# Optimization experiments

Measured on AMD Instinct MI355X. Metric: run time of the kernel, lower is better.

The kernel has to match this reference:

```python
import jax, jax.numpy as jnp
import numpy as np

MODES1 = 16
MODES2 = 16
WIDTH = 64


def spectral_conv2d(x, w):
    # x: [b, ci, n1, n2] real; w: [ci, co, m1, m2, 2] real (re, im)
    b, ci, n1, n2 = x.shape
    co, m1, m2 = w.shape[1], w.shape[2], w.shape[3]
    x_ft = jnp.fft.rfft2(x, norm='ortho')              # [b, ci, n1, n2//2+1] complex
    wc = w[..., 0] + 1j * w[..., 1]                     # [ci, co, m1, m2]
    blk = jnp.einsum('bixy,ioxy->boxy', x_ft[:, :, :m1, :m2], wc)
    out_ft = jnp.zeros((b, co, n1, n2 // 2 + 1), dtype=x_ft.dtype)
    out_ft = out_ft.at[:, :, :m1, :m2].set(blk)
    return jnp.fft.irfft2(out_ft, s=(n1, n2), norm='ortho')


def conv1x1(x, w, bias):
    # x: [b, ci, n1, n2]; w: [co, ci]; bias: [co]
    return jnp.einsum('bixy,oi->boxy', x, w) + bias[None, :, None, None]


def setup_inputs() -> dict:
    key = jax.random.key(0)
    ks = jax.random.split(key, 20)
    B, CIN, N1, N2 = 16, 3, 256, 256
    W = WIDTH
    scale = 1.0 / (W * W)
    inp = {
        'x': jax.random.normal(ks[0], (B, CIN, N1, N2), dtype=jnp.float32),
        'fc0_w': jax.random.normal(ks[1], (W, CIN), dtype=jnp.float32) * 0.1,
        'fc0_b': jnp.zeros((W,), dtype=jnp.float32),
        'sw1': scale * jax.random.normal(ks[2], (W, W, MODES1, MODES2, 2), dtype=jnp.float32),
        'sw2': scale * jax.random.normal(ks[3], (W, W, MODES1, MODES2, 2), dtype=jnp.float32),
        'sw3': scale * jax.random.normal(ks[4], (W, W, MODES1, MODES2, 2), dtype=jnp.float32),
        'sw4': scale * jax.random.normal(ks[5], (W, W, MODES1, MODES2, 2), dtype=jnp.float32),
        'cw1': jax.random.normal(ks[6], (W, W), dtype=jnp.float32) * 0.05,
        'cb1': jnp.zeros((W,), dtype=jnp.float32),
        'cw2': jax.random.normal(ks[7], (W, W), dtype=jnp.float32) * 0.05,
        'cb2': jnp.zeros((W,), dtype=jnp.float32),
        'cw3': jax.random.normal(ks[8], (W, W), dtype=jnp.float32) * 0.05,
        'cb3': jnp.zeros((W,), dtype=jnp.float32),
        'cw4': jax.random.normal(ks[9], (W, W), dtype=jnp.float32) * 0.05,
        'cb4': jnp.zeros((W,), dtype=jnp.float32),
        'fc1_w': jax.random.normal(ks[10], (64, W), dtype=jnp.float32) * 0.05,
        'fc1_b': jnp.zeros((64,), dtype=jnp.float32),
        'fc2_w': jax.random.normal(ks[11], (1, 64), dtype=jnp.float32) * 0.05,
        'fc2_b': jnp.zeros((1,), dtype=jnp.float32),
    }
    return inp


def reference(x, fc0_w, fc0_b, sw1, sw2, sw3, sw4,
              cw1, cb1, cw2, cb2, cw3, cb3, cw4, cb4,
              fc1_w, fc1_b, fc2_w, fc2_b):
    # lift: [b, c, n1, n2] -> channels-last Linear -> [b, width, n1, n2]
    h = jnp.einsum('bcxy,wc->bwxy', x, fc0_w) + fc0_b[None, :, None, None]
    for sw, cw, cb in ((sw1, cw1, cb1), (sw2, cw2, cb2), (sw3, cw3, cb3), (sw4, cw4, cb4)):
        h = jax.nn.gelu(spectral_conv2d(h, sw) + conv1x1(h, cw, cb), approximate=False)
    # projection head (channels-last linears)
    h = jax.nn.gelu(jnp.einsum('bwxy,fw->bfxy', h, fc1_w) + fc1_b[None, :, None, None], approximate=False)
    out = jnp.einsum('bfxy,of->boxy', h, fc2_w) + fc2_b[None, :, None, None]
    return out
```

## Files before the change

### kernel.cpp

```cpp
#include <hip/hip_runtime.h>
#include <math.h>


typedef unsigned int   u32;
typedef unsigned short u16;
typedef __attribute__((ext_vector_type(8))) __bf16 bf16x8;
typedef __attribute__((ext_vector_type(4))) float  f32x4;

constexpr long F1_B  = 134217728;
constexpr long G_B   = 150994944;
constexpr long F2_B  = 167772160;
constexpr long CC_B  = 169869312;
constexpr long WF_B  = 171966464;
constexpr long WXI_B = 171999232;
constexpr long TWF_B = 172032000;
constexpr long BAS_B = 172048384;
constexpr long WSP_B = 172064768;

constexpr int HOP = 76;

union BU { uint2 u2[2]; uint4 u4; bf16x8 v; u16 s[8]; };

__device__ __forceinline__ float gelu_exact(float v) {
    return 0.5f * v * (1.0f + erff(v * 0.70710678118654752440f));
}
__device__ __forceinline__ float bflo(u32 u) { return __uint_as_float(u << 16); }
__device__ __forceinline__ float bfhi(u32 u) { return __uint_as_float(u & 0xffff0000u); }
__device__ __forceinline__ u16 f2bf(float f) {
    u32 u = __float_as_uint(f);
    u += 0x7fffu + ((u >> 16) & 1u);
    return (u16)(u >> 16);
}
__device__ __forceinline__ u32 pack2bf(float a, float b) {
    return (u32)f2bf(a) | ((u32)f2bf(b) << 16);
}

__global__ __launch_bounds__(256) void k_tab(float* __restrict__ wf,
                                             float* __restrict__ wxi,
                                             u16* __restrict__ twf,
                                             u16* __restrict__ bas) {
    const int t = blockIdx.x * 256 + threadIdx.x;
    if (t < 4096) {
        const int y = t >> 4, k = t & 15;
        const int m = (k * y) & 255;
        double s, c; sincospi((double)m / 128.0, &s, &c);
        wf[t * 2] = (float)c; wf[t * 2 + 1] = (float)(-s);
    } else if (t < 8192) {
        const int u = t - 4096;
        const int k1 = u >> 8, x = u & 255;
        const int m = (k1 * x) & 255;
        double s, c; sincospi((double)m / 128.0, &s, &c);
        wxi[u * 2] = (float)c; wxi[u * 2 + 1] = (float)s;
    } else if (t < 16384) {
        const int u = t - 8192;
        const int kc = u >> 8, y = u & 255;
        const int k2 = kc >> 1;
        const int m = (k2 * y) & 255;
        double s, c; sincospi((double)m / 128.0, &s, &c);
        twf[kc * 256 + y] = f2bf((kc & 1) ? (float)(-s) : (float)c);
    } else {
        const int u = t - 16384;
        const int y = u >> 5, kc = u & 31;
        const int k2 = kc >> 1;
        const int m = (k2 * y) & 255;
        double s, c; sincospi((double)m / 128.0, &s, &c);
        const float cc = (k2 == 0) ? 1.0f : 2.0f;
        bas[y * 32 + kc] = f2bf((kc & 1) ? (float)(-cc * s) : (float)(cc * c));
    }
}

__global__ __launch_bounds__(256) void k_wsplit(const float* __restrict__ c1,
                                                const float* __restrict__ c2,
                                                const float* __restrict__ c3,
                                                const float* __restrict__ c4,
                                                const float* __restrict__ f1w,
                                                u16* __restrict__ wsp) {
    const int t = blockIdx.x * 256 + threadIdx.x;
    const int w = t >> 12, p = t & 4095;
    const float* src = (w == 0) ? c1 : (w == 1) ? c2 : (w == 2) ? c3
                     : (w == 3) ? c4 : f1w;
    const float f = src[p];
    const u16 hi = f2bf(f);
    const u16 lo = f2bf(f - __uint_as_float((u32)hi << 16));
    u16* dst = wsp + w * 8192 + (p >> 6) * 128 + (p & 63);
    dst[0]  = hi;
    dst[64] = lo;
}

__device__ __forceinline__ void f1t_epilogue(const u16* HOyo,
                                             const u16* __restrict__ twf,
                                             u16* __restrict__ f1,
                                             int b, int x, int tid) {
    const int lane = tid & 63, wave = tid >> 6;
    const int quad = lane >> 4, col = lane & 15;
    const int o = wave * 16 + col;
    f32x4 a0 = {0.f, 0.f, 0.f, 0.f}, a1 = {0.f, 0.f, 0.f, 0.f};
    #pragma unroll
    for (int ks = 0; ks < 8; ks++) {
        const int kb = ks * 32 + quad * 8;
        BU bb;
        #pragma unroll
        for (int j = 0; j < 8; j++) bb.s[j] = HOyo[(kb + j) * HOP + o];
        const bf16x8 af0 = *(const bf16x8*)(twf + col * 256 + kb);
        const bf16x8 af1 = *(const bf16x8*)(twf + (16 + col) * 256 + kb);
        a0 = __builtin_amdgcn_mfma_f32_16x16x32_bf16(af0, bb.v, a0, 0, 0, 0);
        a1 = __builtin_amdgcn_mfma_f32_16x16x32_bf16(af1, bb.v, a1, 0, 0, 0);
    }
    u16* dst = f1 + (((long)(b * 64 + o)) * 256 + x) * 32 + quad * 4;
    uint2 w;
    w.x = pack2bf(a0[0], a0[1]); w.y = pack2bf(a0[2], a0[3]);
    *(uint2*)dst = w;
    w.x = pack2bf(a1[0], a1[1]); w.y = pack2bf(a1[2], a1[3]);
    *(uint2*)(dst + 16) = w;
}

__global__ __launch_bounds__(256) void k_lift(const float* __restrict__ xin,
                                              const float* __restrict__ w0,
                                              const float* __restrict__ b0,
                                              u16* __restrict__ h,
                                              const u16* __restrict__ twf,
                                              u16* __restrict__ f1) {
    __shared__ float ws0[192], bs0[64];
    __shared__ u16 HOyo[256 * HOP];
    const int tid = threadIdx.x;
    if (tid < 192) ws0[tid] = w0[tid];
    if (tid < 64)  bs0[tid] = b0[tid];
    __syncthreads();
    const int b = blockIdx.x >> 8, x = blockIdx.x & 255;
    const long pix = (((long)b * 3) * 256 + x) * 256 + tid;
    const float x0 = xin[pix];
    const float x1 = xin[pix + 65536];
    const float x2 = xin[pix + 131072];
    u32 pr[32];
    #pragma unroll
    for (int w = 0; w < 64; w += 2) {
        float v0 = bs0[w], v1 = bs0[w + 1];
        v0 = fmaf(x0, ws0[w * 3],     v0);  v1 = fmaf(x0, ws0[w * 3 + 3], v1);
        v0 = fmaf(x1, ws0[w * 3 + 1], v0);  v1 = fmaf(x1, ws0[w * 3 + 4], v1);
        v0 = fmaf(x2, ws0[w * 3 + 2], v0);  v1 = fmaf(x2, ws0[w * 3 + 5], v1);
        pr[w >> 1] = pack2bf(v0, v1);
    }
    u16* hrow = h + (((long)(b * 256 + x)) << 14) + (long)tid * 64;
    #pragma unroll
    for (int q = 0; q < 8; q++) *(uint4*)(hrow + q * 8) = ((uint4*)pr)[q];
    #pragma unroll
    for (int q = 0; q < 16; q++)
        *(uint2*)(HOyo + tid * HOP + q * 4) = ((uint2*)pr)[q];
    __syncthreads();
    f1t_epilogue(HOyo, twf, f1, b, x, tid);
}

__global__ __launch_bounds__(256) void k_dftx(const u16* __restrict__ f1,
                                              const float* __restrict__ wf,
                                              float* __restrict__ f2) {
    const int tid = threadIdx.x;
    const int k1 = tid >> 4, k2 = tid & 15;
    const u16* base = f1 + (long)blockIdx.x * 8192;
    float cr0 = 0, ci0 = 0, cr1 = 0, ci1 = 0;
    for (int x = 0; x < 256; x += 2) {
        const u32 wa = *(const u32*)(base + x * 32 + k2 * 2);
        const float2 ta = *(const float2*)(wf + x * 32 + k1 * 2);
        const float Far = bflo(wa), Fai = bfhi(wa);
        cr0 = fmaf(Far, ta.x, fmaf(-Fai, ta.y, cr0));
        ci0 = fmaf(Fai, ta.x, fmaf(Far, ta.y, ci0));
        const u32 wb = *(const u32*)(base + (x + 1) * 32 + k2 * 2);
        const float2 tb = *(const float2*)(wf + (x + 1) * 32 + k1 * 2);
        const float Fbr = bflo(wb), Fbi = bfhi(wb);
        cr1 = fmaf(Fbr, tb.x, fmaf(-Fbi, tb.y, cr1));
        ci1 = fmaf(Fbi, tb.x, fmaf(Fbr, tb.y, ci1));
    }
    const int m = k1 * 16 + k2;
    *(float2*)(f2 + ((long)m * 1024 + blockIdx.x) * 2) =
        make_float2(cr0 + cr1, ci0 + ci1);
}

__global__ __launch_bounds__(256) void k_mode(const float* __restrict__ f2,
                                              const float* __restrict__ sw,
                                              float* __restrict__ cc) {
    __shared__ __align__(16) float wsh[8192];
    __shared__ __align__(16) float fsh[2048];
    const int tid = threadIdx.x;
    const int m = blockIdx.x;
    const float scale = 1.0f / 65536.0f;
    for (int p = tid; p < 4096; p += 256) {
        const float2 w = *(const float2*)(sw + ((long)p * 256 + m) * 2);
        wsh[p * 2]     = w.x * scale;
        wsh[p * 2 + 1] = w.y * scale;
    }
    for (int t = tid; t < 2048; t += 256) fsh[t] = f2[(long)m * 2048 + t];
    __syncthreads();
    const int b = tid >> 4, o0 = (tid & 15) * 4;
    float re[4] = {0, 0, 0, 0}, im[4] = {0, 0, 0, 0};
    for (int i = 0; i < 64; i++) {
        const float2 F = *(const float2*)(fsh + (b * 64 + i) * 2);
        #pragma unroll
        for (int oo = 0; oo < 4; oo++) {
            const float2 W = *(const float2*)(wsh + (i * 64 + o0 + oo) * 2);
            re[oo] = fmaf(F.x, W.x, fmaf(-F.y, W.y, re[oo]));
            im[oo] = fmaf(F.x, W.y, fmaf(F.y, W.x, im[oo]));
        }
    }
    #pragma unroll
    for (int oo = 0; oo < 4; oo++) {
        *(float2*)(cc + ((long)m * 1024 + b * 64 + o0 + oo) * 2) =
            make_float2(re[oo], im[oo]);
    }
}

__global__ __launch_bounds__(256) void k_invx(const float* __restrict__ cc,
                                              const float* __restrict__ wxi,
                                              u16* __restrict__ g) {
    __shared__ __align__(16) float csh[512];
    const int tid = threadIdx.x;
    const int blk = blockIdx.x;
    ((float2*)csh)[tid] = *(const float2*)(cc + ((long)tid * 1024 + blk) * 2);
    __syncthreads();
    const int x = tid;
    float ar[16], ai[16];
    #pragma unroll
    for (int k = 0; k < 16; k++) { ar[k] = 0; ai[k] = 0; }
    for (int k1 = 0; k1 < 16; k1++) {
        const float2 t = *(const float2*)(wxi + (k1 * 256 + x) * 2);
        #pragma unroll
        for (int k2 = 0; k2 < 16; k2++) {
            const float2 C = ((const float2*)csh)[k1 * 16 + k2];
            ar[k2] = fmaf(C.x, t.x, fmaf(-C.y, t.y, ar[k2]));
            ai[k2] = fmaf(C.x, t.y, fmaf(C.y, t.x, ai[k2]));
        }
    }
    u32 wbuf[16];
    #pragma unroll
    for (int k = 0; k < 16; k++) wbuf[k] = pack2bf(ar[k], ai[k]);
    u16* ob = g + ((long)blk * 256 + x) * 32;
    #pragma unroll
    for (int q = 0; q < 4; q++) *(uint4*)(ob + q * 8) = ((uint4*)wbuf)[q];
}

__device__ __forceinline__ void conv_phase1(const u16* __restrict__ h, long hbase,
                                            const u16* __restrict__ Gbf,
                                            const u16* __restrict__ wsp,
                                            const u16* __restrict__ bas,
                                            int b, int x, int tid, f32x4 (*acc)[4]) {
    const int lane = tid & 63, wave = tid >> 6;
    const int quad = lane >> 4, col = lane & 15;
    #pragma unroll
    for (int ks = 0; ks < 2; ks++) {
        bf16x8 B[4], Ah[4], Al[4];
        #pragma unroll
        for (int nt = 0; nt < 4; nt++) {
            const int y = wave * 64 + nt * 16 + col;
            B[nt] = *(const bf16x8*)(h + hbase + (long)y * 64 + ks * 32 + quad * 8);
        }
        #pragma unroll
        for (int mt = 0; mt < 4; mt++) {
            Ah[mt] = *(const bf16x8*)(wsp + (mt * 16 + col) * 128 + ks * 32 + quad * 8);
            Al[mt] = *(const bf16x8*)(wsp + (mt * 16 + col) * 128 + 64 + ks * 32 + quad * 8);
        }
        #pragma unroll
        for (int mt = 0; mt < 4; mt++)
            #pragma unroll
            for (int nt = 0; nt < 4; nt++) {
                acc[mt][nt] = __builtin_amdgcn_mfma_f32_16x16x32_bf16(Ah[mt], B[nt], acc[mt][nt], 0, 0, 0);
                acc[mt][nt] = __builtin_amdgcn_mfma_f32_16x16x32_bf16(Al[mt], B[nt], acc[mt][nt], 0, 0, 0);
            }
    }
    {
        bf16x8 B[4], Ag[4];
        #pragma unroll
        for (int nt = 0; nt < 4; nt++) {
            const int y = wave * 64 + nt * 16 + col;
            B[nt] = *(const bf16x8*)(bas + y * 32 + quad * 8);
        }
        #pragma unroll
        for (int mt = 0; mt < 4; mt++)
            Ag[mt] = *(const bf16x8*)(Gbf + (((long)(b * 64 + mt * 16 + col)) * 256 + x) * 32 + quad * 8);
        #pragma unroll
        for (int mt = 0; mt < 4; mt++)
            #pragma unroll
            for (int nt = 0; nt < 4; nt++)
                acc[mt][nt] = __builtin_amdgcn_mfma_f32_16x16x32_bf16(Ag[mt], B[nt], acc[mt][nt], 0, 0, 0);
    }
}

__global__ __launch_bounds__(256, 3) void k_conv(u16* __restrict__ h,
                                                 const u16* __restrict__ Gbf,
                                                 const u16* __restrict__ wsp,
                                                 const float* __restrict__ cb,
                                                 const u16* __restrict__ bas,
                                                 const u16* __restrict__ twf,
                                                 u16* __restrict__ f1) {
    __shared__ u16 HOyo[256 * HOP];
    __shared__ float cbs[64];
    const int tid = threadIdx.x;
    const int b = blockIdx.x >> 8, x = blockIdx.x & 255;
    const long hbase = ((long)(b * 256 + x)) << 14;
    if (tid < 64) cbs[tid] = cb[tid];
    f32x4 acc[4][4];
    const f32x4 z = {0.f, 0.f, 0.f, 0.f};
    #pragma unroll
    for (int i = 0; i < 4; i++)
        #pragma unroll
        for (int j = 0; j < 4; j++) acc[i][j] = z;
    conv_phase1(h, hbase, Gbf, wsp, bas, b, x, tid, acc);
    __syncthreads();
    const int lane = tid & 63, wave = tid >> 6;
    const int quad = lane >> 4, col = lane & 15;
    #pragma unroll
    for (int mt = 0; mt < 4; mt++) {
        const int o0 = mt * 16 + quad * 4;
        const float c0 = cbs[o0], c1 = cbs[o0 + 1], c2 = cbs[o0 + 2], c3 = cbs[o0 + 3];
        #pragma unroll
        for (int nt = 0; nt < 4; nt++) {
            const int y = wave * 64 + nt * 16 + col;
            uint2 w;
            w.x = pack2bf(gelu_exact(acc[mt][nt][0] + c0), gelu_exact(acc[mt][nt][1] + c1));
            w.y = pack2bf(gelu_exact(acc[mt][nt][2] + c2), gelu_exact(acc[mt][nt][3] + c3));
            *(uint2*)(h + hbase + (long)y * 64 + o0) = w;
            *(uint2*)(HOyo + y * HOP + o0) = w;
        }
    }
    __syncthreads();
    f1t_epilogue(HOyo, twf, f1, b, x, tid);
}

__global__ __launch_bounds__(256, 3) void k_conv_head(const u16* __restrict__ h,
                                                      const u16* __restrict__ Gbf,
                                                      const u16* __restrict__ wsp,
                                                      const float* __restrict__ cb,
                                                      const u16* __restrict__ bas,
                                                      const u16* __restrict__ w1sp,
                                                      const float* __restrict__ b1,
                                                      const float* __restrict__ w2,
                                                      const float* __restrict__ b2,
                                                      float* __restrict__ out) {
    __shared__ u16 HOyo[256 * HOP];
    __shared__ float cbs[64], b1s[64], w2s[64];
    const int tid = threadIdx.x;
    const int b = blockIdx.x >> 8, x = blockIdx.x & 255;
    const long hbase = ((long)(b * 256 + x)) << 14;
    if (tid < 64) { cbs[tid] = cb[tid]; b1s[tid] = b1[tid]; w2s[tid] = w2[tid]; }
    const float bias2 = b2[0];
    f32x4 acc[4][4];
    const f32x4 z = {0.f, 0.f, 0.f, 0.f};
    #pragma unroll
    for (int i = 0; i < 4; i++)
        #pragma unroll
        for (int j = 0; j < 4; j++) acc[i][j] = z;
    conv_phase1(h, hbase, Gbf, wsp, bas, b, x, tid, acc);
    __syncthreads();
    const int lane = tid & 63, wave = tid >> 6;
    const int quad = lane >> 4, col = lane & 15;
    #pragma unroll
    for (int mt = 0; mt < 4; mt++) {
        const int o0 = mt * 16 + quad * 4;
        const float c0 = cbs[o0], c1 = cbs[o0 + 1], c2 = cbs[o0 + 2], c3 = cbs[o0 + 3];
        #pragma unroll
        for (int nt = 0; nt < 4; nt++) {
            const int y = wave * 64 + nt * 16 + col;
            uint2 w;
            w.x = pack2bf(gelu_exact(acc[mt][nt][0] + c0), gelu_exact(acc[mt][nt][1] + c1));
            w.y = pack2bf(gelu_exact(acc[mt][nt][2] + c2), gelu_exact(acc[mt][nt][3] + c3));
            *(uint2*)(HOyo + y * HOP + o0) = w;
        }
    }
    __syncthreads();
    f32x4 acc2[4][4];
    #pragma unroll
    for (int i = 0; i < 4; i++)
        #pragma unroll
        for (int j = 0; j < 4; j++) acc2[i][j] = z;
    #pragma unroll
    for (int ks = 0; ks < 4; ks++) {
        const int kk = (ks & 1) * 32 + quad * 8;
        bf16x8 B[4], A[4];
        #pragma unroll
        for (int nt = 0; nt < 4; nt++) {
            const int y = wave * 64 + nt * 16 + col;
            BU bb;
            bb.u2[0] = *(const uint2*)(HOyo + y * HOP + kk);
            bb.u2[1] = *(const uint2*)(HOyo + y * HOP + kk + 4);
            B[nt] = bb.v;
        }
        #pragma unroll
        for (int mt = 0; mt < 4; mt++)
            A[mt] = *(const bf16x8*)(w1sp + (mt * 16 + col) * 128 + ks * 32 + quad * 8);
        #pragma unroll
        for (int mt = 0; mt < 4; mt++)
            #pragma unroll
            for (int nt = 0; nt < 4; nt++)
                acc2[mt][nt] = __builtin_amdgcn_mfma_f32_16x16x32_bf16(A[mt], B[nt], acc2[mt][nt], 0, 0, 0);
    }
    float p4[4] = {0.f, 0.f, 0.f, 0.f};
    #pragma unroll
    for (int mt = 0; mt < 4; mt++)
        #pragma unroll
        for (int r = 0; r < 4; r++) {
            const int f = mt * 16 + quad * 4 + r;
            const float bb = b1s[f], ww = w2s[f];
            #pragma unroll
            for (int nt = 0; nt < 4; nt++)
                p4[nt] = fmaf(ww, gelu_exact(acc2[mt][nt][r] + bb), p4[nt]);
        }
    #pragma unroll
    for (int nt = 0; nt < 4; nt++) {
        p4[nt] += __shfl_xor(p4[nt], 16);
        p4[nt] += __shfl_xor(p4[nt], 32);
    }
    out[(long)b * 65536 + x * 256 + wave * 64 + lane] = p4[quad] + bias2;
}

extern "C" void kernel_launch(void* const* d_in, const int* in_sizes, int n_in,
                              void* d_out, int out_size, void* d_ws, size_t ws_size,
                              hipStream_t stream) {
    const float* x     = (const float*)d_in[0];
    const float* fc0_w = (const float*)d_in[1];
    const float* fc0_b = (const float*)d_in[2];
    const float* sw[4] = {(const float*)d_in[3], (const float*)d_in[4],
                          (const float*)d_in[5], (const float*)d_in[6]};
    const float* cwA[4] = {(const float*)d_in[7],  (const float*)d_in[9],
                           (const float*)d_in[11], (const float*)d_in[13]};
    const float* cbA[4] = {(const float*)d_in[8],  (const float*)d_in[10],
                           (const float*)d_in[12], (const float*)d_in[14]};
    const float* fc1_w = (const float*)d_in[15];
    const float* fc1_b = (const float*)d_in[16];
    const float* fc2_w = (const float*)d_in[17];
    const float* fc2_b = (const float*)d_in[18];

    char* base = (char*)d_ws;
    u16*   h    = (u16*)base;
    u16*   f1   = (u16*)(base + F1_B);
    u16*   Gbf  = (u16*)(base + G_B);
    float* f2   = (float*)(base + F2_B);
    float* cbuf = (float*)(base + CC_B);
    float* wf   = (float*)(base + WF_B);
    float* wxi  = (float*)(base + WXI_B);
    u16*   twf  = (u16*)(base + TWF_B);
    u16*   bas  = (u16*)(base + BAS_B);
    u16*   wsp  = (u16*)(base + WSP_B);

    k_tab<<<96, 256, 0, stream>>>(wf, wxi, twf, bas);
    k_wsplit<<<80, 256, 0, stream>>>(cwA[0], cwA[1], cwA[2], cwA[3], fc1_w, wsp);
    k_lift<<<4096, 256, 0, stream>>>(x, fc0_w, fc0_b, h, twf, f1);
    for (int l = 0; l < 4; l++) {
        k_dftx<<<1024, 256, 0, stream>>>(f1, wf, f2);
        k_mode<<<256, 256, 0, stream>>>(f2, sw[l], cbuf);
        k_invx<<<1024, 256, 0, stream>>>(cbuf, wxi, Gbf);
        if (l < 3) {
            k_conv<<<4096, 256, 0, stream>>>(h, Gbf, wsp + l * 8192, cbA[l],
                                             bas, twf, f1);
        } else {
            k_conv_head<<<4096, 256, 0, stream>>>(h, Gbf, wsp + 3 * 8192, cbA[3],
                                                  bas, wsp + 4 * 8192, fc1_b,
                                                  fc2_w, fc2_b, (float*)d_out);
        }
    }
}
```

Measured before the change: 984.9 us.

## Coalesce G layout and h writeback, drop bias smem staging, raise occupancy

Reorders the spectral-inverse G buffer to [b][x][o][k] so each conv block reads a contiguous slab, and rewrites the h store to go through shared memory as coalesced 128-byte rows per thread. Bias, b1 and w2 are now read directly from global as float4 instead of staged in shared memory, which removes one __syncthreads. The launch bound for k_conv is raised to 4 blocks per CU, which may force register spills.

```diff
diff --git a/kernel.cpp b/kernel.cpp
--- a/kernel.cpp
+++ b/kernel.cpp
@@ -213,6 +213,7 @@
     __shared__ __align__(16) float csh[512];
     const int tid = threadIdx.x;
     const int blk = blockIdx.x;
+    const int b = blk >> 6, o = blk & 63;
     ((float2*)csh)[tid] = *(const float2*)(cc + ((long)tid * 1024 + blk) * 2);
     __syncthreads();
     const int x = tid;
@@ -231,7 +232,7 @@
     u32 wbuf[16];
     #pragma unroll
     for (int k = 0; k < 16; k++) wbuf[k] = pack2bf(ar[k], ai[k]);
-    u16* ob = g + ((long)blk * 256 + x) * 32;
+    u16* ob = g + (((long)(b * 256 + x)) * 64 + o) * 32;
     #pragma unroll
     for (int q = 0; q < 4; q++) *(uint4*)(ob + q * 8) = ((uint4*)wbuf)[q];
 }
@@ -273,7 +274,7 @@
         }
         #pragma unroll
         for (int mt = 0; mt < 4; mt++)
-            Ag[mt] = *(const bf16x8*)(Gbf + (((long)(b * 64 + mt * 16 + col)) * 256 + x) * 32 + quad * 8);
+            Ag[mt] = *(const bf16x8*)(Gbf + (((long)(b * 256 + x)) * 64 + mt * 16 + col) * 32 + quad * 8);
         #pragma unroll
         for (int mt = 0; mt < 4; mt++)
             #pragma unroll
@@ -282,7 +283,7 @@
     }
 }
 
-__global__ __launch_bounds__(256, 3) void k_conv(u16* __restrict__ h,
+__global__ __launch_bounds__(256, 4) void k_conv(u16* __restrict__ h,
                                                  const u16* __restrict__ Gbf,
                                                  const u16* __restrict__ wsp,
                                                  const float* __restrict__ cb,
@@ -290,11 +291,9 @@
                                                  const u16* __restrict__ twf,
                                                  u16* __restrict__ f1) {
     __shared__ u16 HOyo[256 * HOP];
-    __shared__ float cbs[64];
     const int tid = threadIdx.x;
     const int b = blockIdx.x >> 8, x = blockIdx.x & 255;
     const long hbase = ((long)(b * 256 + x)) << 14;
-    if (tid < 64) cbs[tid] = cb[tid];
     f32x4 acc[4][4];
     const f32x4 z = {0.f, 0.f, 0.f, 0.f};
     #pragma unroll
@@ -302,24 +301,31 @@
         #pragma unroll
         for (int j = 0; j < 4; j++) acc[i][j] = z;
     conv_phase1(h, hbase, Gbf, wsp, bas, b, x, tid, acc);
-    __syncthreads();
     const int lane = tid & 63, wave = tid >> 6;
     const int quad = lane >> 4, col = lane & 15;
     #pragma unroll
     for (int mt = 0; mt < 4; mt++) {
         const int o0 = mt * 16 + quad * 4;
-        const float c0 = cbs[o0], c1 = cbs[o0 + 1], c2 = cbs[o0 + 2], c3 = cbs[o0 + 3];
+        const float4 cbv = *(const float4*)(cb + o0);
         #pragma unroll
         for (int nt = 0; nt < 4; nt++) {
             const int y = wave * 64 + nt * 16 + col;
             uint2 w;
-            w.x = pack2bf(gelu_exact(acc[mt][nt][0] + c0), gelu_exact(acc[mt][nt][1] + c1));
-            w.y = pack2bf(gelu_exact(acc[mt][nt][2] + c2), gelu_exact(acc[mt][nt][3] + c3));
-            *(uint2*)(h + hbase + (long)y * 64 + o0) = w;
+            w.x = pack2bf(gelu_exact(acc[mt][nt][0] + cbv.x), gelu_exact(acc[mt][nt][1] + cbv.y));
+            w.y = pack2bf(gelu_exact(acc[mt][nt][2] + cbv.z), gelu_exact(acc[mt][nt][3] + cbv.w));
             *(uint2*)(HOyo + y * HOP + o0) = w;
         }
     }
     __syncthreads();
+    {
+        uint2 tmp[16];
+        const u16* sr = HOyo + tid * HOP;
+        #pragma unroll
+        for (int k = 0; k < 16; k++) tmp[k] = *(const uint2*)(sr + k * 4);
+        u16* dh = h + hbase + (long)tid * 64;
+        #pragma unroll
+        for (int q = 0; q < 8; q++) *(uint4*)(dh + q * 8) = ((uint4*)tmp)[q];
+    }
     f1t_epilogue(HOyo, twf, f1, b, x, tid);
 }
 
@@ -334,11 +340,9 @@
                                                       const float* __restrict__ b2,
                                                       float* __restrict__ out) {
     __shared__ u16 HOyo[256 * HOP];
-    __shared__ float cbs[64], b1s[64], w2s[64];
     const int tid = threadIdx.x;
     const int b = blockIdx.x >> 8, x = blockIdx.x & 255;
     const long hbase = ((long)(b * 256 + x)) << 14;
-    if (tid < 64) { cbs[tid] = cb[tid]; b1s[tid] = b1[tid]; w2s[tid] = w2[tid]; }
     const float bias2 = b2[0];
     f32x4 acc[4][4];
     const f32x4 z = {0.f, 0.f, 0.f, 0.f};
@@ -347,19 +351,18 @@
         #pragma unroll
         for (int j = 0; j < 4; j++) acc[i][j] = z;
     conv_phase1(h, hbase, Gbf, wsp, bas, b, x, tid, acc);
-    __syncthreads();
     const int lane = tid & 63, wave = tid >> 6;
     const int quad = lane >> 4, col = lane & 15;
     #pragma unroll
     for (int mt = 0; mt < 4; mt++) {
         const int o0 = mt * 16 + quad * 4;
-        const float c0 = cbs[o0], c1 = cbs[o0 + 1], c2 = cbs[o0 + 2], c3 = cbs[o0 + 3];
+        const float4 cbv = *(const float4*)(cb + o0);
         #pragma unroll
         for (int nt = 0; nt < 4; nt++) {
             const int y = wave * 64 + nt * 16 + col;
             uint2 w;
-            w.x = pack2bf(gelu_exact(acc[mt][nt][0] + c0), gelu_exact(acc[mt][nt][1] + c1));
-            w.y = pack2bf(gelu_exact(acc[mt][nt][2] + c2), gelu_exact(acc[mt][nt][3] + c3));
+            w.x = pack2bf(gelu_exact(acc[mt][nt][0] + cbv.x), gelu_exact(acc[mt][nt][1] + cbv.y));
+            w.y = pack2bf(gelu_exact(acc[mt][nt][2] + cbv.z), gelu_exact(acc[mt][nt][3] + cbv.w));
             *(uint2*)(HOyo + y * HOP + o0) = w;
         }
     }
@@ -392,15 +395,19 @@
     }
     float p4[4] = {0.f, 0.f, 0.f, 0.f};
     #pragma unroll
-    for (int mt = 0; mt < 4; mt++)
+    for (int mt = 0; mt < 4; mt++) {
+        const int f0 = mt * 16 + quad * 4;
+        const float4 b1v = *(const float4*)(b1 + f0);
+        const float4 w2v = *(const float4*)(w2 + f0);
         #pragma unroll
         for (int r = 0; r < 4; r++) {
-            const int f = mt * 16 + quad * 4 + r;
-            const float bb = b1s[f], ww = w2s[f];
+            const float bb = (&b1v.x)[r];
+            const float ww = (&w2v.x)[r];
             #pragma unroll
             for (int nt = 0; nt < 4; nt++)
                 p4[nt] = fmaf(ww, gelu_exact(acc2[mt][nt][r] + bb), p4[nt]);
         }
+    }
     #pragma unroll
     for (int nt = 0; nt < 4; nt++) {
         p4[nt] += __shfl_xor(p4[nt], 16);
```

Result: slower. 1.061 ms (+7.7%).
